# Performance work log

Hardware: AMD Instinct MI355X
Metric: run time of the kernel (lower is better)

The kernel has to match this reference:

```python
import jax, jax.numpy as jnp
import numpy as np

NFEAT = 256
N_HEAD = 8
CTXS = (31, 61)
HPS = N_HEAD // len(CTXS)  # heads per scale = 4


def _scale_out(query, value, W1, W2, W3, ctx):
    # query, value: [B, T, F]; W1: [F, F]; W2: [F, HPS*ctx]; W3: [F, F]
    B, T, F = query.shape
    q = jnp.maximum(query @ W1, 0.0)                      # relu(w1(query))
    attn = jax.nn.softmax((q @ W2).reshape(B, T, HPS, ctx), axis=-1)  # [B,T,HPS,ctx]
    half = (ctx - 1) // 2
    v = jnp.pad(value @ W3, ((0, 0), (half, half), (0, 0)))  # [B, T+ctx-1, F]
    idx = jnp.arange(T)[:, None] + jnp.arange(ctx)[None, :]  # [T, ctx] window indices
    vw = v[:, idx]                                          # [B, T, ctx, F]
    vw = vw.reshape(B, T, ctx, HPS, F // HPS)               # per-head dim = F/HPS
    out = jnp.einsum('bthc,btchd->bthd', attn, vw)          # [B,T,HPS,F/HPS]
    return out.reshape(B, T, F)


def setup_inputs() -> dict:
    key = jax.random.key(0)
    ks = jax.random.split(key, 12)
    B, T, F = 2, 4096, NFEAT
    s = 0.02
    return {
        'query': jax.random.normal(ks[0], (B, T, F), jnp.float32),
        'key':   jax.random.normal(ks[1], (B, T, F), jnp.float32),
        'value': jax.random.normal(ks[2], (B, T, F), jnp.float32),
        'w1_0': jax.random.normal(ks[3], (F, F), jnp.float32) * s,
        'w1_1': jax.random.normal(ks[4], (F, F), jnp.float32) * s,
        'w2_0': jax.random.normal(ks[5], (F, HPS * CTXS[0]), jnp.float32) * s,
        'w2_1': jax.random.normal(ks[6], (F, HPS * CTXS[1]), jnp.float32) * s,
        'w3_0': jax.random.normal(ks[7], (F, F), jnp.float32) * s,
        'w3_1': jax.random.normal(ks[8], (F, F), jnp.float32) * s,
        'scale_w': jnp.ones((2,), jnp.float32) / 2.0,
        'w_out': jax.random.normal(ks[9], (F, F), jnp.float32) * s,
    }


def reference(query, key, value, w1_0, w1_1, w2_0, w2_1, w3_0, w3_1, scale_w, w_out):
    sw = jax.nn.softmax(scale_w)
    out = sw[0] * _scale_out(query, value, w1_0, w2_0, w3_0, CTXS[0])
    out = out + sw[1] * _scale_out(query, value, w1_1, w2_1, w3_1, CTXS[1])
    return out @ w_out
```

## Files before the change

### kernel.cpp

```cpp
#include <hip/hip_runtime.h>
#include <hip/hip_bf16.h>
#include <type_traits>

static constexpr int BATCH = 2;
static constexpr int T     = 4096;
static constexpr int F     = 256;
static constexpr int M     = BATCH * T;
static constexpr int HPS   = 4;
static constexpr int CTX0  = 31, CTX1 = 61;
static constexpr int LGN   = 384;

typedef short bf16x8 __attribute__((ext_vector_type(8)));
typedef float f32x4  __attribute__((ext_vector_type(4)));

__device__ __forceinline__ ushort f2bf(float f) {
    union { float f; uint u; } v; v.f = f;
    uint u = v.u;
    return (ushort)((u + 0x7fffu + ((u >> 16) & 1u)) >> 16);
}
__device__ __forceinline__ float asf(uint u) {
    union { uint u; float f; } v; v.u = u; return v.f;
}
__device__ __forceinline__ float bf2f(ushort u) { return asf(((uint)u) << 16); }

static constexpr size_t W1T_OFF  = 0;
static constexpr size_t W2B_OFF  = W1T_OFF + (size_t)512 * 256;
static constexpr size_t W3T_OFF  = W2B_OFF + (size_t)384 * 512;
static constexpr size_t WOT_OFF  = W3T_OFF + (size_t)512 * 256;
static constexpr size_t WT_ELEMS = WOT_OFF + (size_t)256 * 256;

struct WcvtArgs {
    const float* w1_0; const float* w1_1;
    const float* w2_0; const float* w2_1;
    const float* w3_0; const float* w3_1;
    const float* wo;
    ushort* wt;
};

__global__ __launch_bounds__(256) void wcvt_kernel(WcvtArgs a) {
    int gid = blockIdx.x * 256 + threadIdx.x;
    if (gid >= (int)(WT_ELEMS / 8)) return;
    ushort o[8];
    if (gid < 16384 || (gid >= 16384 + 24576 && gid < 16384 + 24576 + 16384)) {
        bool w3 = gid >= 16384;
        int g = w3 ? gid - (16384 + 24576) : gid;
        int row = g >> 5;
        int kk  = (g & 31) * 8;
        const float* src = (row < 256) ? (w3 ? a.w3_0 : a.w1_0) : (w3 ? a.w3_1 : a.w1_1);
        int col = row & 255;
#pragma unroll
        for (int j = 0; j < 8; j++) o[j] = f2bf(src[(size_t)(kk + j) * 256 + col]);
        size_t base = (w3 ? W3T_OFF : W1T_OFF) + (size_t)row * 256 + kk;
        *reinterpret_cast<bf16x8*>(a.wt + base) = *reinterpret_cast<bf16x8*>(o);
    } else if (gid < 16384 + 24576) {
        int g = gid - 16384;
        int row = g >> 6;
        int kk  = (g & 63) * 8;
#pragma unroll
        for (int j = 0; j < 8; j++) {
            int k = kk + j;
            float v = 0.f;
            if (row < 124) { if (k < 256) v = a.w2_0[(size_t)k * 124 + row]; }
            else if (row < 368) { if (k >= 256) v = a.w2_1[(size_t)(k - 256) * 244 + (row - 124)]; }
            o[j] = f2bf(v);
        }
        *reinterpret_cast<bf16x8*>(a.wt + W2B_OFF + (size_t)row * 512 + kk) =
            *reinterpret_cast<bf16x8*>(o);
    } else {
        int g = gid - (16384 + 24576 + 16384);
        int row = g >> 5;
        int kk  = (g & 31) * 8;
#pragma unroll
        for (int j = 0; j < 8; j++) o[j] = f2bf(a.wo[(size_t)(kk + j) * 256 + row]);
        *reinterpret_cast<bf16x8*>(a.wt + WOT_OFF + (size_t)row * 256 + kk) =
            *reinterpret_cast<bf16x8*>(o);
    }
}

template <int KTOT, int AMODE, typename OutT, bool RELU>
__global__ __launch_bounds__(256, 4) void gemm_kernel(
    const void* __restrict__ Av, const void* __restrict__ A2v, int lda,
    const ushort* __restrict__ Bt,
    OutT* __restrict__ C, int N, int ncb)
{
    __shared__ ushort Al[64][128];
    __shared__ ushort Bl[64][128];

    const int tid = threadIdx.x;
    const int nwg = gridDim.x;
    const int lin = blockIdx.x;
    const int qq  = nwg >> 3;
    const int swz = (lin & 7) * qq + (lin >> 3);
    const int cb  = swz % ncb;
    const int rb  = swz / ncb;
    const int m0  = rb * 64;
    const int n0  = cb * 64;

    const ushort* Ab  = (const ushort*)Av;
    const float*  Af  = (const float*)Av;
    const ushort* A2b = (const ushort*)A2v;

    const int wave = tid >> 6, lane = tid & 63;
    const int wr = wave >> 1, wc = wave & 1;
    const int l15 = lane & 15, l4 = lane >> 4;

    f32x4 acc[2][2] = {};

    for (int kh = 0; kh < KTOT / 128; kh++) {
#pragma unroll
        for (int it = 0; it < 4; it++) {
            int i = it * 256 + tid;
            int row = i >> 4, ch = i & 15;
            int k = kh * 128 + ch * 8;
            bf16x8 v;
            if constexpr (AMODE == 0) {
                v = *reinterpret_cast<const bf16x8*>(Ab + (size_t)(m0 + row) * lda + k);
            } else if constexpr (AMODE == 1) {
                const float* ap = Af + (size_t)(m0 + row) * lda + k;
                float4 x = *reinterpret_cast<const float4*>(ap);
                float4 y = *reinterpret_cast<const float4*>(ap + 4);
                ushort o[8] = { f2bf(x.x), f2bf(x.y), f2bf(x.z), f2bf(x.w),
                                f2bf(y.x), f2bf(y.y), f2bf(y.z), f2bf(y.w) };
                v = *reinterpret_cast<bf16x8*>(o);
            } else {
                bf16x8 p = *reinterpret_cast<const bf16x8*>(Ab  + (size_t)(m0 + row) * lda + k);
                bf16x8 q = *reinterpret_cast<const bf16x8*>(A2b + (size_t)(m0 + row) * lda + k);
                ushort o[8];
#pragma unroll
                for (int j = 0; j < 8; j++)
                    o[j] = f2bf(bf2f((ushort)p[j]) + bf2f((ushort)q[j]));
                v = *reinterpret_cast<bf16x8*>(o);
            }
            *reinterpret_cast<bf16x8*>(&Al[row][(ch ^ (row & 7)) * 8]) = v;
        }
#pragma unroll
        for (int it = 0; it < 4; it++) {
            int i = it * 256 + tid;
            int row = i >> 4, ch = i & 15;
            int k = kh * 128 + ch * 8;
            bf16x8 v = *reinterpret_cast<const bf16x8*>(Bt + (size_t)(n0 + row) * KTOT + k);
            *reinterpret_cast<bf16x8*>(&Bl[row][(ch ^ (row & 7)) * 8]) = v;
        }
        __syncthreads();

#pragma unroll
        for (int s = 0; s < 4; s++) {
            bf16x8 af[2], bfr[2];
#pragma unroll
            for (int i = 0; i < 2; i++) {
                int row = wr * 32 + i * 16 + l15;
                int ch  = (s * 4 + l4) ^ (row & 7);
                af[i] = *reinterpret_cast<const bf16x8*>(&Al[row][ch * 8]);
            }
#pragma unroll
            for (int j = 0; j < 2; j++) {
                int row = wc * 32 + j * 16 + l15;
                int ch  = (s * 4 + l4) ^ (row & 7);
                bfr[j] = *reinterpret_cast<const bf16x8*>(&Bl[row][ch * 8]);
            }
#pragma unroll
            for (int i = 0; i < 2; i++)
#pragma unroll
                for (int j = 0; j < 2; j++)
                    acc[i][j] = __builtin_amdgcn_mfma_f32_16x16x32_bf16(af[i], bfr[j], acc[i][j], 0, 0, 0);
        }
        __syncthreads();
    }

#pragma unroll
    for (int i = 0; i < 2; i++)
#pragma unroll
        for (int j = 0; j < 2; j++) {
            int col = n0 + wc * 32 + j * 16 + l15;
#pragma unroll
            for (int r = 0; r < 4; r++) {
                int row = m0 + wr * 32 + i * 16 + l4 * 4 + r;
                float v = acc[i][j][r];
                if (RELU) v = fmaxf(v, 0.0f);
                if constexpr (std::is_same<OutT, ushort>::value)
                    C[(size_t)row * N + col] = f2bf(v);
                else
                    C[(size_t)row * N + col] = v;
            }
        }
}

template <int SCALE>
__global__ __launch_bounds__(256) void attn_kernel(
    const float*  __restrict__ lg,
    const ushort* __restrict__ v01,
    const float*  __restrict__ scale_w,
    ushort*       __restrict__ p)
{
    constexpr int CTX  = SCALE ? CTX1 : CTX0;
    constexpr int HALO = (CTX - 1) / 2;
    constexpr int VR   = 32 + 2 * HALO;
    constexpr int LGO  = SCALE ? 124 : 0;
    constexpr int VOFF = SCALE ? 256 : 0;

    __shared__ ushort vl[VR][256];
    __shared__ float  att[32][HPS * CTX];

    const int tid = threadIdx.x;
    const int nwg = gridDim.x;
    const int lin = blockIdx.x;
    const int qq  = nwg >> 3;
    const int swz = (lin & 7) * qq + (lin >> 3);
    const int bt0 = swz * 32;
    const int b   = bt0 >> 12;
    const int t0  = bt0 & (T - 1);

    for (int i = tid; i < VR * 32; i += 256) {
        int row = i >> 5, ch = i & 31;
        int tt = t0 - HALO + row;
        bf16x8 v = {};
        if ((unsigned)tt < (unsigned)T)
            v = *reinterpret_cast<const bf16x8*>(
                v01 + ((size_t)(b * T + tt) * 512 + VOFF + ch * 8));
        *reinterpret_cast<bf16x8*>(&vl[row][ch * 8]) = v;
    }

    float s0 = scale_w[0], s1 = scale_w[1];
    float mxs = fmaxf(s0, s1);
    float e0 = __expf(s0 - mxs), e1 = __expf(s1 - mxs);
    float sw = (SCALE ? e1 : e0) / (e0 + e1);

    {
        int task = tid >> 1, sub = tid & 1;
        int tok = task >> 2, h = task & 3;
        const float* lp = lg + (size_t)(bt0 + tok) * LGN + LGO + h * CTX;
        float* dst = &att[tok][h * CTX];
        float mx = -1e30f;
        for (int c = sub; c < CTX; c += 2) mx = fmaxf(mx, lp[c]);
        mx = fmaxf(mx, __shfl_xor(mx, 1));
        float s = 0.f;
        for (int c = sub; c < CTX; c += 2) {
            float e = __expf(lp[c] - mx);
            dst[c] = e; s += e;
        }
        s += __shfl_xor(s, 1);
        float scl = sw / s;
        for (int c = sub; c < CTX; c += 2) dst[c] *= scl;
    }
    __syncthreads();

    const int w  = tid >> 5;
    const int f0 = (tid & 31) * 8;
    const int h  = f0 >> 6;

#pragma unroll 1
    for (int tk = 0; tk < 4; tk++) {
        int tok = tk * 8 + w;
        const float* aw = &att[tok][h * CTX];
        float acc[8] = {};
#pragma unroll 4
        for (int c = 0; c < CTX; c++) {
            float wv = aw[c];
            uint4 u = *reinterpret_cast<const uint4*>(&vl[tok + c][f0]);
            acc[0] += wv * asf(u.x << 16); acc[1] += wv * asf(u.x & 0xffff0000u);
            acc[2] += wv * asf(u.y << 16); acc[3] += wv * asf(u.y & 0xffff0000u);
            acc[4] += wv * asf(u.z << 16); acc[5] += wv * asf(u.z & 0xffff0000u);
            acc[6] += wv * asf(u.w << 16); acc[7] += wv * asf(u.w & 0xffff0000u);
        }
        ushort o[8];
#pragma unroll
        for (int j = 0; j < 8; j++) o[j] = f2bf(acc[j]);
        *reinterpret_cast<bf16x8*>(p + (size_t)(bt0 + tok) * F + f0) =
            *reinterpret_cast<bf16x8*>(o);
    }
}

extern "C" void kernel_launch(void* const* d_in, const int* in_sizes, int n_in,
                              void* d_out, int out_size, void* d_ws, size_t ws_size,
                              hipStream_t stream)
{
    const float* Q    = (const float*)d_in[0];
    const float* V    = (const float*)d_in[2];
    const float* W1_0 = (const float*)d_in[3];
    const float* W1_1 = (const float*)d_in[4];
    const float* W2_0 = (const float*)d_in[5];
    const float* W2_1 = (const float*)d_in[6];
    const float* W3_0 = (const float*)d_in[7];
    const float* W3_1 = (const float*)d_in[8];
    const float* SW   = (const float*)d_in[9];
    const float* WO   = (const float*)d_in[10];

    char* pws = (char*)d_ws;
    auto carve = [&](size_t bytes) { char* r = pws; pws += (bytes + 255) & ~255ull; return r; };
    ushort* wt  = (ushort*)carve(WT_ELEMS * 2);
    ushort* q01 = (ushort*)carve((size_t)M * 512 * 2);
    float*  lg  = (float*) carve((size_t)M * LGN * 4);
    ushort* v01 = (ushort*)carve((size_t)M * 512 * 2);
    ushort* p0  = (ushort*)carve((size_t)M * F * 2);
    ushort* p1  = (ushort*)carve((size_t)M * F * 2);
    (void)ws_size;

    const ushort* w1t   = wt + W1T_OFF;
    const ushort* w2blk = wt + W2B_OFF;
    const ushort* w3t   = wt + W3T_OFF;
    const ushort* wot   = wt + WOT_OFF;

    wcvt_kernel<<<(int)(WT_ELEMS / 8 / 256), 256, 0, stream>>>(
        WcvtArgs{ W1_0, W1_1, W2_0, W2_1, W3_0, W3_1, WO, wt });

    gemm_kernel<256, 1, ushort, true ><<<(M/64) * 8, 256, 0, stream>>>(
        Q, nullptr, 256, w1t, q01, 512, 8);
    gemm_kernel<256, 1, ushort, false><<<(M/64) * 8, 256, 0, stream>>>(
        V, nullptr, 256, w3t, v01, 512, 8);
    gemm_kernel<512, 0, float,  false><<<(M/64) * 6, 256, 0, stream>>>(
        q01, nullptr, 512, w2blk, lg, LGN, 6);
    attn_kernel<0><<<M / 32, 256, 0, stream>>>(lg, v01, SW, p0);
    attn_kernel<1><<<M / 32, 256, 0, stream>>>(lg, v01, SW, p1);
    gemm_kernel<256, 2, float,  false><<<(M/64) * 4, 256, 0, stream>>>(
        p0, p1, 256, wot, (float*)d_out, 256, 4);
}
```

Before: 159.1 us.

## Use 128x128 double-buffered GEMM tiles and merge launches into fewer kernels

Replaces the 64x64 GEMM with a 128x128 tile kernel that prefetches the next K-slice into registers and double-buffers LDS, for more reuse per load and loads that overlap the MFMA work. The Q and V projections are merged into one launch, the two attention scales into one launch, and weight conversion now transposes through shared memory for coalesced reads. The larger tiles cut the block count to 128-512 on a GPU with many CUs, which may leave compute units idle, and the higher register use lowers occupancy.

Result: faster. 140.5 us (-11.7%).

```diff
diff --git a/kernel.cpp b/kernel.cpp
--- a/kernel.cpp
+++ b/kernel.cpp
@@ -2,13 +2,12 @@
 #include <hip/hip_bf16.h>
 #include <type_traits>
 
-static constexpr int BATCH = 2;
-static constexpr int T     = 4096;
-static constexpr int F     = 256;
-static constexpr int M     = BATCH * T;
-static constexpr int HPS   = 4;
-static constexpr int CTX0  = 31, CTX1 = 61;
-static constexpr int LGN   = 384;
+static constexpr int T    = 4096;
+static constexpr int F    = 256;
+static constexpr int M    = 2 * T;
+static constexpr int HPS  = 4;
+static constexpr int CTX0 = 31, CTX1 = 61;
+static constexpr int LGN  = 384;
 
 typedef short bf16x8 __attribute__((ext_vector_type(8)));
 typedef float f32x4  __attribute__((ext_vector_type(4)));
@@ -29,7 +28,7 @@
 static constexpr size_t WOT_OFF  = W3T_OFF + (size_t)512 * 256;
 static constexpr size_t WT_ELEMS = WOT_OFF + (size_t)256 * 256;
 
-struct WcvtArgs {
+struct WArgs {
     const float* w1_0; const float* w1_1;
     const float* w2_0; const float* w2_1;
     const float* w3_0; const float* w3_1;
@@ -37,146 +36,204 @@
     ushort* wt;
 };
 
-__global__ __launch_bounds__(256) void wcvt_kernel(WcvtArgs a) {
-    int gid = blockIdx.x * 256 + threadIdx.x;
-    if (gid >= (int)(WT_ELEMS / 8)) return;
-    ushort o[8];
-    if (gid < 16384 || (gid >= 16384 + 24576 && gid < 16384 + 24576 + 16384)) {
-        bool w3 = gid >= 16384;
-        int g = w3 ? gid - (16384 + 24576) : gid;
-        int row = g >> 5;
-        int kk  = (g & 31) * 8;
-        const float* src = (row < 256) ? (w3 ? a.w3_0 : a.w1_0) : (w3 ? a.w3_1 : a.w1_1);
-        int col = row & 255;
-#pragma unroll
-        for (int j = 0; j < 8; j++) o[j] = f2bf(src[(size_t)(kk + j) * 256 + col]);
-        size_t base = (w3 ? W3T_OFF : W1T_OFF) + (size_t)row * 256 + kk;
-        *reinterpret_cast<bf16x8*>(a.wt + base) = *reinterpret_cast<bf16x8*>(o);
-    } else if (gid < 16384 + 24576) {
-        int g = gid - 16384;
-        int row = g >> 6;
-        int kk  = (g & 63) * 8;
-#pragma unroll
-        for (int j = 0; j < 8; j++) {
-            int k = kk + j;
-            float v = 0.f;
-            if (row < 124) { if (k < 256) v = a.w2_0[(size_t)k * 124 + row]; }
-            else if (row < 368) { if (k >= 256) v = a.w2_1[(size_t)(k - 256) * 244 + (row - 124)]; }
-            o[j] = f2bf(v);
-        }
-        *reinterpret_cast<bf16x8*>(a.wt + W2B_OFF + (size_t)row * 512 + kk) =
+__global__ __launch_bounds__(256) void wprep_kernel(WArgs a) {
+    __shared__ float tb[64][72];
+    const int tid = threadIdx.x;
+    const int blk = blockIdx.x;
+
+    const float* src = nullptr;
+    ushort* dst; int dstLD, k0, nbase; bool isw2 = false;
+
+    if (blk < 64) {
+        int sec = blk >> 4;
+        int tt = blk & 15, kt = tt >> 2, nt = tt & 3;
+        k0 = kt * 64;
+        src = (sec == 0) ? a.w1_0 : (sec == 1) ? a.w1_1 : (sec == 2) ? a.w3_0 : a.w3_1;
+        dst = a.wt + ((sec < 2) ? W1T_OFF : W3T_OFF);
+        nbase = (sec & 1) * 256 + nt * 64;
+        dstLD = 256;
+    } else if (blk < 80) {
+        int tt = blk - 64, kt = tt >> 2, nt = tt & 3;
+        k0 = kt * 64; src = a.wo; dst = a.wt + WOT_OFF; nbase = nt * 64; dstLD = 256;
+    } else {
+        int tt = blk - 80;
+        int nt = tt >> 3, kt = tt & 7;
+        k0 = kt * 64; nbase = nt * 64; dst = a.wt + W2B_OFF; dstLD = 512; isw2 = true;
+    }
+
+    {
+        int kk = tid >> 2;
+        int c4 = (tid & 3) * 16;
+        if (!isw2) {
+            int ncol0 = (blk < 64) ? (nbase & 255) : nbase;
+            const float* sp = src + (size_t)(k0 + kk) * 256 + ncol0 + c4;
+#pragma unroll
+            for (int ii = 0; ii < 4; ii++) {
+                float4 v = *reinterpret_cast<const float4*>(sp + ii * 4);
+                tb[kk][c4 + ii * 4 + 0] = v.x; tb[kk][c4 + ii * 4 + 1] = v.y;
+                tb[kk][c4 + ii * 4 + 2] = v.z; tb[kk][c4 + ii * 4 + 3] = v.w;
+            }
+        } else {
+            int k = k0 + kk;
+#pragma unroll 4
+            for (int ii = 0; ii < 16; ii++) {
+                int n = nbase + c4 + ii;
+                float v = 0.f;
+                if (n < 124) { if (k < 256) v = a.w2_0[(size_t)k * 124 + n]; }
+                else if (n < 368) { if (k >= 256) v = a.w2_1[(size_t)(k - 256) * 244 + (n - 124)]; }
+                tb[kk][c4 + ii] = v;
+            }
+        }
+    }
+    __syncthreads();
+
+#pragma unroll
+    for (int it = 0; it < 2; it++) {
+        int slot = it * 256 + tid;
+        int n = slot >> 3, ch = slot & 7;
+        ushort o[8];
+#pragma unroll
+        for (int j = 0; j < 8; j++) o[j] = f2bf(tb[ch * 8 + j][n]);
+        *reinterpret_cast<bf16x8*>(dst + (size_t)(nbase + n) * dstLD + k0 + ch * 8) =
             *reinterpret_cast<bf16x8*>(o);
-    } else {
-        int g = gid - (16384 + 24576 + 16384);
-        int row = g >> 5;
-        int kk  = (g & 31) * 8;
-#pragma unroll
-        for (int j = 0; j < 8; j++) o[j] = f2bf(a.wo[(size_t)(kk + j) * 256 + row]);
-        *reinterpret_cast<bf16x8*>(a.wt + WOT_OFF + (size_t)row * 256 + kk) =
-            *reinterpret_cast<bf16x8*>(o);
-    }
-}
-
-template <int KTOT, int AMODE, typename OutT, bool RELU>
-__global__ __launch_bounds__(256, 4) void gemm_kernel(
-    const void* __restrict__ Av, const void* __restrict__ A2v, int lda,
-    const ushort* __restrict__ Bt,
-    OutT* __restrict__ C, int N, int ncb)
-{
-    __shared__ ushort Al[64][128];
-    __shared__ ushort Bl[64][128];
+    }
+}
+
+struct GemmArgs {
+    const void* A0; const void* A1; const void* A2;
+    const ushort* B0; const ushort* B1;
+    void* C0; void* C1;
+    int lda, N, ncb, relu0, relu1;
+};
+
+template <int KTOT, int AMODE, int NPAIR, typename OutT>
+__global__ __launch_bounds__(256, 2) void gemm128_kernel(GemmArgs a) {
+    __shared__ ushort Al[2][128][64];
+    __shared__ ushort Bl[2][128][64];
 
     const int tid = threadIdx.x;
-    const int nwg = gridDim.x;
-    const int lin = blockIdx.x;
-    const int qq  = nwg >> 3;
+    int lin = blockIdx.x;
+    int half = gridDim.x;
+    int sel = 0;
+    if constexpr (NPAIR == 2) {
+        half >>= 1;
+        sel = lin >= half;
+        lin -= sel * half;
+    }
+    const int qq  = half >> 3;
     const int swz = (lin & 7) * qq + (lin >> 3);
-    const int cb  = swz % ncb;
-    const int rb  = swz / ncb;
-    const int m0  = rb * 64;
-    const int n0  = cb * 64;
-
-    const ushort* Ab  = (const ushort*)Av;
-    const float*  Af  = (const float*)Av;
-    const ushort* A2b = (const ushort*)A2v;
+    const int cb  = swz % a.ncb;
+    const int rb  = swz / a.ncb;
+    const int m0  = rb * 128;
+    const int n0  = cb * 128;
+
+    const void*   Av  = sel ? a.A1 : a.A0;
+    const ushort* Bt  = sel ? a.B1 : a.B0;
+    OutT*         C   = (OutT*)(sel ? a.C1 : a.C0);
+    const bool    relu = sel ? (a.relu1 != 0) : (a.relu0 != 0);
+    const int     lda = a.lda, N = a.N;
 
     const int wave = tid >> 6, lane = tid & 63;
     const int wr = wave >> 1, wc = wave & 1;
     const int l15 = lane & 15, l4 = lane >> 4;
-
-    f32x4 acc[2][2] = {};
-
-    for (int kh = 0; kh < KTOT / 128; kh++) {
+    const int srow = tid >> 3;
+    const int sch  = tid & 7;
+
+    float4 pAf[4][2];
+    bf16x8 pAb[4];
+    bf16x8 pA2[4];
+    bf16x8 pB[4];
+
+    auto loadRegs = [&](int s) {
+        const int k0 = s * 64;
 #pragma unroll
         for (int it = 0; it < 4; it++) {
-            int i = it * 256 + tid;
-            int row = i >> 4, ch = i & 15;
-            int k = kh * 128 + ch * 8;
-            bf16x8 v;
-            if constexpr (AMODE == 0) {
-                v = *reinterpret_cast<const bf16x8*>(Ab + (size_t)(m0 + row) * lda + k);
-            } else if constexpr (AMODE == 1) {
-                const float* ap = Af + (size_t)(m0 + row) * lda + k;
-                float4 x = *reinterpret_cast<const float4*>(ap);
-                float4 y = *reinterpret_cast<const float4*>(ap + 4);
-                ushort o[8] = { f2bf(x.x), f2bf(x.y), f2bf(x.z), f2bf(x.w),
-                                f2bf(y.x), f2bf(y.y), f2bf(y.z), f2bf(y.w) };
-                v = *reinterpret_cast<bf16x8*>(o);
+            int row = it * 32 + srow;
+            if constexpr (AMODE == 1) {
+                const float* ap = (const float*)Av + (size_t)(m0 + row) * lda + k0 + sch * 8;
+                pAf[it][0] = *reinterpret_cast<const float4*>(ap);
+                pAf[it][1] = *reinterpret_cast<const float4*>(ap + 4);
             } else {
-                bf16x8 p = *reinterpret_cast<const bf16x8*>(Ab  + (size_t)(m0 + row) * lda + k);
-                bf16x8 q = *reinterpret_cast<const bf16x8*>(A2b + (size_t)(m0 + row) * lda + k);
+                pAb[it] = *reinterpret_cast<const bf16x8*>(
+                    (const ushort*)Av + (size_t)(m0 + row) * lda + k0 + sch * 8);
+                if constexpr (AMODE == 2)
+                    pA2[it] = *reinterpret_cast<const bf16x8*>(
+                        (const ushort*)a.A2 + (size_t)(m0 + row) * lda + k0 + sch * 8);
+            }
+            pB[it] = *reinterpret_cast<const bf16x8*>(
+                Bt + (size_t)(n0 + row) * KTOT + k0 + sch * 8);
+        }
+    };
+    auto writeLds = [&](int buf) {
+#pragma unroll
+        for (int it = 0; it < 4; it++) {
+            int row = it * 32 + srow;
+            int c8  = (sch ^ (row & 7)) * 8;
+            bf16x8 av;
+            if constexpr (AMODE == 1) {
+                ushort o[8] = { f2bf(pAf[it][0].x), f2bf(pAf[it][0].y),
+                                f2bf(pAf[it][0].z), f2bf(pAf[it][0].w),
+                                f2bf(pAf[it][1].x), f2bf(pAf[it][1].y),
+                                f2bf(pAf[it][1].z), f2bf(pAf[it][1].w) };
+                av = *reinterpret_cast<bf16x8*>(o);
+            } else if constexpr (AMODE == 2) {
                 ushort o[8];
 #pragma unroll
                 for (int j = 0; j < 8; j++)
-                    o[j] = f2bf(bf2f((ushort)p[j]) + bf2f((ushort)q[j]));
-                v = *reinterpret_cast<bf16x8*>(o);
-            }
-            *reinterpret_cast<bf16x8*>(&Al[row][(ch ^ (row & 7)) * 8]) = v;
-        }
-#pragma unroll
-        for (int it = 0; it < 4; it++) {
-            int i = it * 256 + tid;
-            int row = i >> 4, ch = i & 15;
-            int k = kh * 128 + ch * 8;
-            bf16x8 v = *reinterpret_cast<const bf16x8*>(Bt + (size_t)(n0 + row) * KTOT + k);
-            *reinterpret_cast<bf16x8*>(&Bl[row][(ch ^ (row & 7)) * 8]) = v;
-        }
+                    o[j] = f2bf(bf2f((ushort)pAb[it][j]) + bf2f((ushort)pA2[it][j]));
+                av = *reinterpret_cast<bf16x8*>(o);
+            } else {
+                av = pAb[it];
+            }
+            *reinterpret_cast<bf16x8*>(&Al[buf][row][c8]) = av;
+            *reinterpret_cast<bf16x8*>(&Bl[buf][row][c8]) = pB[it];
+        }
+    };
+
+    f32x4 acc[4][4] = {};
+
+    loadRegs(0);
+    writeLds(0);
+    constexpr int NST = KTOT / 64;
+#pragma unroll
+    for (int s = 0; s < NST; s++) {
+        if (s + 1 < NST) loadRegs(s + 1);
         __syncthreads();
-
-#pragma unroll
-        for (int s = 0; s < 4; s++) {
-            bf16x8 af[2], bfr[2];
-#pragma unroll
-            for (int i = 0; i < 2; i++) {
-                int row = wr * 32 + i * 16 + l15;
-                int ch  = (s * 4 + l4) ^ (row & 7);
-                af[i] = *reinterpret_cast<const bf16x8*>(&Al[row][ch * 8]);
-            }
-#pragma unroll
-            for (int j = 0; j < 2; j++) {
-                int row = wc * 32 + j * 16 + l15;
-                int ch  = (s * 4 + l4) ^ (row & 7);
-                bfr[j] = *reinterpret_cast<const bf16x8*>(&Bl[row][ch * 8]);
-            }
-#pragma unroll
-            for (int i = 0; i < 2; i++)
-#pragma unroll
-                for (int j = 0; j < 2; j++)
-                    acc[i][j] = __builtin_amdgcn_mfma_f32_16x16x32_bf16(af[i], bfr[j], acc[i][j], 0, 0, 0);
-        }
-        __syncthreads();
-    }
-
-#pragma unroll
-    for (int i = 0; i < 2; i++)
-#pragma unroll
-        for (int j = 0; j < 2; j++) {
-            int col = n0 + wc * 32 + j * 16 + l15;
+        if (s + 1 < NST) writeLds((s + 1) & 1);
+        const int buf = s & 1;
+#pragma unroll
+        for (int ks = 0; ks < 2; ks++) {
+            bf16x8 af[4], bv[4];
+#pragma unroll
+            for (int i = 0; i < 4; i++) {
+                int row = wr * 64 + i * 16 + l15;
+                int ch  = (ks * 4 + l4) ^ (row & 7);
+                af[i] = *reinterpret_cast<const bf16x8*>(&Al[buf][row][ch * 8]);
+            }
+#pragma unroll
+            for (int j = 0; j < 4; j++) {
+                int row = wc * 64 + j * 16 + l15;
+                int ch  = (ks * 4 + l4) ^ (row & 7);
+                bv[j] = *reinterpret_cast<const bf16x8*>(&Bl[buf][row][ch * 8]);
+            }
+#pragma unroll
+            for (int i = 0; i < 4; i++)
+#pragma unroll
+                for (int j = 0; j < 4; j++)
+                    acc[i][j] = __builtin_amdgcn_mfma_f32_16x16x32_bf16(af[i], bv[j], acc[i][j], 0, 0, 0);
+        }
+    }
+
+#pragma unroll
+    for (int i = 0; i < 4; i++)
+#pragma unroll
+        for (int j = 0; j < 4; j++) {
+            int col = n0 + wc * 64 + j * 16 + l15;
 #pragma unroll
             for (int r = 0; r < 4; r++) {
-                int row = m0 + wr * 32 + i * 16 + l4 * 4 + r;
+                int row = m0 + wr * 64 + i * 16 + l4 * 4 + r;
                 float v = acc[i][j][r];
-                if (RELU) v = fmaxf(v, 0.0f);
+                if (relu) v = fmaxf(v, 0.0f);
                 if constexpr (std::is_same<OutT, ushort>::value)
                     C[(size_t)row * N + col] = f2bf(v);
                 else
@@ -185,30 +242,33 @@
         }
 }
 
-template <int SCALE>
 __global__ __launch_bounds__(256) void attn_kernel(
     const float*  __restrict__ lg,
     const ushort* __restrict__ v01,
     const float*  __restrict__ scale_w,
-    ushort*       __restrict__ p)
+    ushort*       __restrict__ p0,
+    ushort*       __restrict__ p1)
 {
-    constexpr int CTX  = SCALE ? CTX1 : CTX0;
-    constexpr int HALO = (CTX - 1) / 2;
-    constexpr int VR   = 32 + 2 * HALO;
-    constexpr int LGO  = SCALE ? 124 : 0;
-    constexpr int VOFF = SCALE ? 256 : 0;
-
-    __shared__ ushort vl[VR][256];
-    __shared__ float  att[32][HPS * CTX];
-
-    const int tid = threadIdx.x;
-    const int nwg = gridDim.x;
-    const int lin = blockIdx.x;
-    const int qq  = nwg >> 3;
+    __shared__ ushort vl[92][256];
+    __shared__ float  att[32][HPS * CTX1];
+
+    const int tid  = threadIdx.x;
+    const int half = gridDim.x >> 1;
+    int lin = blockIdx.x;
+    const int sc = lin >= half;
+    lin -= sc * half;
+    const int qq  = half >> 3;
     const int swz = (lin & 7) * qq + (lin >> 3);
     const int bt0 = swz * 32;
     const int b   = bt0 >> 12;
     const int t0  = bt0 & (T - 1);
+
+    const int CTX  = sc ? CTX1 : CTX0;
+    const int HALO = (CTX - 1) >> 1;
+    const int VR   = 32 + 2 * HALO;
+    const int LGO  = sc ? 124 : 0;
+    const int VOFF = sc ? 256 : 0;
+    ushort* p = sc ? p1 : p0;
 
     for (int i = tid; i < VR * 32; i += 256) {
         int row = i >> 5, ch = i & 31;
@@ -223,7 +283,7 @@
     float s0 = scale_w[0], s1 = scale_w[1];
     float mxs = fmaxf(s0, s1);
     float e0 = __expf(s0 - mxs), e1 = __expf(s1 - mxs);
-    float sw = (SCALE ? e1 : e0) / (e0 + e1);
+    float sw = (sc ? e1 : e0) / (e0 + e1);
 
     {
         int task = tid >> 1, sub = tid & 1;
@@ -300,17 +360,28 @@
     const ushort* w3t   = wt + W3T_OFF;
     const ushort* wot   = wt + WOT_OFF;
 
-    wcvt_kernel<<<(int)(WT_ELEMS / 8 / 256), 256, 0, stream>>>(
-        WcvtArgs{ W1_0, W1_1, W2_0, W2_1, W3_0, W3_1, WO, wt });
-
-    gemm_kernel<256, 1, ushort, true ><<<(M/64) * 8, 256, 0, stream>>>(
-        Q, nullptr, 256, w1t, q01, 512, 8);
-    gemm_kernel<256, 1, ushort, false><<<(M/64) * 8, 256, 0, stream>>>(
-        V, nullptr, 256, w3t, v01, 512, 8);
-    gemm_kernel<512, 0, float,  false><<<(M/64) * 6, 256, 0, stream>>>(
-        q01, nullptr, 512, w2blk, lg, LGN, 6);
-    attn_kernel<0><<<M / 32, 256, 0, stream>>>(lg, v01, SW, p0);
-    attn_kernel<1><<<M / 32, 256, 0, stream>>>(lg, v01, SW, p1);
-    gemm_kernel<256, 2, float,  false><<<(M/64) * 4, 256, 0, stream>>>(
-        p0, p1, 256, wot, (float*)d_out, 256, 4);
-}
+    wprep_kernel<<<128, 256, 0, stream>>>(
+        WArgs{ W1_0, W1_1, W2_0, W2_1, W3_0, W3_1, WO, wt });
+
+    {
+        GemmArgs ga{};
+        ga.A0 = Q;  ga.A1 = V;  ga.A2 = nullptr;
+        ga.B0 = w1t; ga.B1 = w3t;
+        ga.C0 = q01; ga.C1 = v01;
+        ga.lda = 256; ga.N = 512; ga.ncb = 4; ga.relu0 = 1; ga.relu1 = 0;
+        gemm128_kernel<256, 1, 2, ushort><<<512, 256, 0, stream>>>(ga);
+    }
+    {
+        GemmArgs ga{};
+        ga.A0 = q01; ga.B0 = w2blk; ga.C0 = lg;
+        ga.lda = 512; ga.N = LGN; ga.ncb = 3; ga.relu0 = 0;
+        gemm128_kernel<512, 0, 1, float><<<192, 256, 0, stream>>>(ga);
+    }
+    attn_kernel<<<512, 256, 0, stream>>>(lg, v01, SW, p0, p1);
+    {
+        GemmArgs ga{};
+        ga.A0 = p0; ga.A2 = p1; ga.B0 = wot; ga.C0 = d_out;
+        ga.lda = 256; ga.N = 256; ga.ncb = 2; ga.relu0 = 0;
+        gemm128_kernel<256, 2, 1, float><<<128, 256, 0, stream>>>(ga);
+    }
+}
```
